# Optimization experiments

Measured on AMD Instinct MI355X. Metric: run time of the kernel, lower is better.

The kernel has to match this reference:

```python
import jax, jax.numpy as jnp
import numpy as np

SCALE = 0.125  # 1/sqrt(d_k), d_k = 64


def setup_inputs() -> dict:
    key = jax.random.key(0)
    kq, kk, kv, kp = jax.random.split(key, 4)
    H, B, L, T, D = 16, 4, 1024, 1024, 64
    return {
        "query": jax.random.normal(kq, (H, B, L, D), dtype=jnp.float32),
        "key": jax.random.normal(kk, (H, B, T, D), dtype=jnp.float32),
        "value": jax.random.normal(kv, (H, B, T, D), dtype=jnp.float32),
        "prev_attention": jax.random.normal(kp, (H, B, L, T), dtype=jnp.float32),
    }


def reference(query, key, value, prev_attention):
    # scores: [h, b, l, t]
    scores = jnp.einsum("hblk,hbtk->hblt", query, key) * SCALE
    scores = scores + prev_attention
    attention = jax.nn.softmax(scores, axis=-1)
    # dropout disabled (rate 0.0) for deterministic reference
    output = jnp.einsum("hblt,hbtv->hblv", attention, value)
    return (output, attention)
```

## Files before the change

### kernel.cpp

```cpp
#include <hip/hip_runtime.h>

#define SCALE 0.125f

constexpr int L_ = 1024, T_ = 1024, D_ = 64, HB_ = 64, QB = 16;

using f32x4  = __attribute__((ext_vector_type(4))) float;
using half8  = __attribute__((ext_vector_type(8))) _Float16;
using half4  = __attribute__((ext_vector_type(4))) _Float16;
using half2v = __attribute__((ext_vector_type(2))) _Float16;

#define BARRIER() asm volatile("s_waitcnt lgkmcnt(0)\n\ts_barrier" ::: "memory")

__global__ __launch_bounds__(256, 3) void attn_fused(
    const float* __restrict__ q, const float* __restrict__ kk,
    const float* __restrict__ vv, const float* __restrict__ prev,
    float* __restrict__ out, float* __restrict__ att) {
  __shared__ __align__(16) _Float16 El[QB][1032];
  __shared__ __align__(16) unsigned char KV[18432];
  __shared__ float zb[4][16];

  auto Ks  = (_Float16(*)[72])KV;
  auto Vt  = (_Float16(*)[72])(KV + 9216);
  auto ob4 = (float(*)[16][72])KV;

  const int ltile = blockIdx.x;
  const int hb    = blockIdx.y;
  const int tid = threadIdx.x;
  const int w = tid >> 6, l = tid & 63, l15 = l & 15, lg = l >> 4;
  const int qrow = ltile * QB + l15;

  half8 qb2[2];
  {
    const float* qp = q + ((size_t)hb * L_ + qrow) * D_ + lg * 8;
#pragma unroll
    for (int f = 0; f < 2; ++f)
#pragma unroll
      for (int e = 0; e < 8; ++e) qb2[f][e] = (_Float16)qp[f * 32 + e];
  }

  const float* prow =
      prev + ((size_t)hb * L_ + qrow) * (size_t)T_ + w * 16 + lg * 4;
  const float* kbase = kk + (size_t)hb * T_ * D_;
  const float* vbase = vv + (size_t)hb * T_ * D_;

  const int sr = tid >> 2;
  const int sc = (tid & 3) * 16;
  const int sv_d = (tid & 15) * 4;
  const int sv_t = (tid >> 4) * 4;

  f32x4 kq[2][4], vq[2][4];
  f32x4 pbv[2];
  auto kload = [&](int c, int s) {
    const float* p = kbase + (size_t)(c * 64 + sr) * D_ + sc;
#pragma unroll
    for (int i = 0; i < 4; ++i) kq[s][i] = *(const f32x4*)(p + i * 4);
  };
  auto vload = [&](int c, int s) {
    const float* p = vbase + (size_t)(c * 64 + sv_t) * D_ + sv_d;
#pragma unroll
    for (int j = 0; j < 4; ++j) vq[s][j] = *(const f32x4*)(p + j * D_);
  };
  auto pload = [&](int c, int s) { pbv[s] = *(const f32x4*)(prow + c * 64); };
  auto kwrite = [&](int s) {
    half8 h0, h1;
#pragma unroll
    for (int e = 0; e < 4; ++e) {
      h0[e]     = (_Float16)kq[s][0][e];
      h0[4 + e] = (_Float16)kq[s][1][e];
      h1[e]     = (_Float16)kq[s][2][e];
      h1[4 + e] = (_Float16)kq[s][3][e];
    }
    *(half8*)&Ks[sr][sc] = h0;
    *(half8*)&Ks[sr][sc + 8] = h1;
  };
  auto vwrite = [&](int s) {
#pragma unroll
    for (int dd = 0; dd < 4; ++dd) {
      half2v a, b;
      a[0] = (_Float16)vq[s][0][dd]; a[1] = (_Float16)vq[s][1][dd];
      b[0] = (_Float16)vq[s][2][dd]; b[1] = (_Float16)vq[s][3][dd];
      *(half2v*)&Vt[sv_d + dd][sv_t]     = a;
      *(half2v*)&Vt[sv_d + dd][sv_t + 2] = b;
    }
  };

  kload(0, 0); vload(0, 0); pload(0, 0);
  kwrite(0); vwrite(0);
  kload(1, 1); vload(1, 1); pload(1, 1);

  float zsum = 0.f;
  f32x4 oacc[4];
#pragma unroll
  for (int nd = 0; nd < 4; ++nd) oacc[nd] = (f32x4){0.f, 0.f, 0.f, 0.f};

#pragma unroll 2
  for (int c = 0; c < 16; ++c) {
    BARRIER();
    f32x4 pv = pbv[c & 1];
    if (c < 14) {
      kload(c + 2, c & 1);
      vload(c + 2, c & 1);
      pload(c + 2, c & 1);
    }

    __builtin_amdgcn_s_setprio(1);
    const int trow = w * 16 + l15;
    half8 ka0 = *(const half8*)&Ks[trow][lg * 8];
    half8 ka1 = *(const half8*)&Ks[trow][32 + lg * 8];
    f32x4 acc = {0.f, 0.f, 0.f, 0.f};
    acc = __builtin_amdgcn_mfma_f32_16x16x32_f16(ka0, qb2[0], acc, 0, 0, 0);
    acc = __builtin_amdgcn_mfma_f32_16x16x32_f16(ka1, qb2[1], acc, 0, 0, 0);

    float e0 = __expf(acc[0] * SCALE + pv[0]);
    float e1 = __expf(acc[1] * SCALE + pv[1]);
    float e2 = __expf(acc[2] * SCALE + pv[2]);
    float e3 = __expf(acc[3] * SCALE + pv[3]);
    zsum += (e0 + e1) + (e2 + e3);
    half4 ev;
    ev[0] = (_Float16)e0; ev[1] = (_Float16)e1;
    ev[2] = (_Float16)e2; ev[3] = (_Float16)e3;
    *(half4*)&El[l15][c * 64 + w * 16 + lg * 4] = ev;

    half8 af;
    af[0] = ev[0]; af[1] = ev[1]; af[2] = ev[2]; af[3] = ev[3];
    af[4] = af[5] = af[6] = af[7] = (_Float16)0.f;
#pragma unroll
    for (int nd = 0; nd < 4; ++nd) {
      half4 v4 = *(const half4*)&Vt[nd * 16 + l15][w * 16 + lg * 4];
      half8 vb;
      vb[0] = v4[0]; vb[1] = v4[1]; vb[2] = v4[2]; vb[3] = v4[3];
      vb[4] = vb[5] = vb[6] = vb[7] = (_Float16)0.f;
      oacc[nd] = __builtin_amdgcn_mfma_f32_16x16x32_f16(af, vb, oacc[nd], 0, 0, 0);
    }
    __builtin_amdgcn_s_setprio(0);

    BARRIER();
    if (c < 15) { kwrite((c + 1) & 1); vwrite((c + 1) & 1); }
  }

  zsum += __shfl_xor(zsum, 16, 64);
  zsum += __shfl_xor(zsum, 32, 64);
  if (lg == 0) zb[w][l15] = zsum;

#pragma unroll
  for (int nd = 0; nd < 4; ++nd)
#pragma unroll
    for (int i = 0; i < 4; ++i)
      ob4[w][lg * 4 + i][nd * 16 + l15] = oacc[nd][i];
  __syncthreads();

  {
    const int qq = tid >> 4, dd = (tid & 15) * 4;
    const float z = (zb[0][qq] + zb[1][qq]) + (zb[2][qq] + zb[3][qq]);
    const float rzq = 1.0f / z;
    f32x4 o0 = *(const f32x4*)&ob4[0][qq][dd];
    f32x4 o1 = *(const f32x4*)&ob4[1][qq][dd];
    f32x4 o2 = *(const f32x4*)&ob4[2][qq][dd];
    f32x4 o3 = *(const f32x4*)&ob4[3][qq][dd];
    f32x4 o = ((o0 + o1) + (o2 + o3));
    o[0] *= rzq; o[1] *= rzq; o[2] *= rzq; o[3] *= rzq;
    *(f32x4*)(out + ((size_t)hb * L_ + ltile * QB + qq) * (size_t)D_ + dd) = o;
  }

  {
    const int row = tid >> 4, tc = tid & 15;
    const float z = (zb[0][row] + zb[1][row]) + (zb[2][row] + zb[3][row]);
    const float rzr = 1.0f / z;
    float* attw =
        att + ((size_t)hb * L_ + ltile * QB + row) * (size_t)T_ + tc * 4;
    const _Float16* ep = &El[row][tc * 4];
#pragma unroll
    for (int j = 0; j < 16; ++j) {
      half4 ev = *(const half4*)(ep + j * 64);
      f32x4 s = {(float)ev[0] * rzr, (float)ev[1] * rzr,
                 (float)ev[2] * rzr, (float)ev[3] * rzr};
      *(f32x4*)(attw + j * 64) = s;
    }
  }
}

extern "C" void kernel_launch(void* const* d_in, const int* in_sizes, int n_in,
                              void* d_out, int out_size, void* d_ws,
                              size_t ws_size, hipStream_t stream) {
  const float* q    = (const float*)d_in[0];
  const float* k    = (const float*)d_in[1];
  const float* v    = (const float*)d_in[2];
  const float* prev = (const float*)d_in[3];

  float* out = (float*)d_out;
  float* att = out + (size_t)HB_ * L_ * D_;

  dim3 grid(L_ / QB, HB_);
  attn_fused<<<grid, 256, 0, stream>>>(q, k, v, prev, out, att);
}
```

Before: 248.5 us.

## Pre-convert K/V to fp16 in workspace and stream directly without LDS staging

Adds two pre-pass kernels that convert K to fp16 and V to a transposed fp16 layout in the workspace. The main kernel then reads K and V fragments straight from global memory (expected to hit L2) instead of staging them through shared memory, which removes the per-chunk barriers and LDS writes. The prev-attention prefetch is restructured into groups of four chunks. The trade-off is extra kernel launches and a workspace round-trip, plus dependence on L2/cache hit rates for the uncoalesced direct loads. The old fused kernel stays as a fallback when the workspace is too small.

```diff
diff --git a/kernel.cpp b/kernel.cpp
--- a/kernel.cpp
+++ b/kernel.cpp
@@ -11,17 +11,54 @@
 
 #define BARRIER() asm volatile("s_waitcnt lgkmcnt(0)\n\ts_barrier" ::: "memory")
 
-__global__ __launch_bounds__(256, 3) void attn_fused(
-    const float* __restrict__ q, const float* __restrict__ kk,
-    const float* __restrict__ vv, const float* __restrict__ prev,
+__global__ __launch_bounds__(256) void cvt_k(const float* __restrict__ k,
+                                             _Float16* __restrict__ kh) {
+  const size_t i = ((size_t)blockIdx.x * 256 + threadIdx.x) * 8;
+  f32x4 a = *(const f32x4*)(k + i);
+  f32x4 b = *(const f32x4*)(k + i + 4);
+  half8 h;
+#pragma unroll
+  for (int e = 0; e < 4; ++e) {
+    h[e] = (_Float16)a[e];
+    h[4 + e] = (_Float16)b[e];
+  }
+  *(half8*)(kh + i) = h;
+}
+
+__global__ __launch_bounds__(256) void cvt_v(const float* __restrict__ v,
+                                             _Float16* __restrict__ vh) {
+  __shared__ _Float16 ts[64][136];
+  const int tid = threadIdx.x;
+  const int hb = blockIdx.y;
+  const int t0 = blockIdx.x * 128;
+
+  {
+    const int tr = tid >> 1, dh = (tid & 1) * 32;
+    const float* p = v + ((size_t)hb * T_ + t0 + tr) * D_ + dh;
+#pragma unroll
+    for (int i = 0; i < 8; ++i) {
+      f32x4 r = *(const f32x4*)(p + i * 4);
+#pragma unroll
+      for (int e = 0; e < 4; ++e) ts[dh + i * 4 + e][tr] = (_Float16)r[e];
+    }
+  }
+  __syncthreads();
+  {
+    const int d = tid >> 2, tq = (tid & 3) * 32;
+    _Float16* qo = vh + ((size_t)hb * D_ + d) * T_ + t0 + tq;
+#pragma unroll
+    for (int i = 0; i < 4; ++i)
+      *(half8*)(qo + i * 8) = *(const half8*)&ts[d][tq + i * 8];
+  }
+}
+
+__global__ __launch_bounds__(256, 3) void attn_stream(
+    const float* __restrict__ q, const _Float16* __restrict__ Kh,
+    const _Float16* __restrict__ Vh, const float* __restrict__ prev,
     float* __restrict__ out, float* __restrict__ att) {
   __shared__ __align__(16) _Float16 El[QB][1032];
-  __shared__ __align__(16) unsigned char KV[18432];
-  __shared__ float zb[4][16];
-
-  auto Ks  = (_Float16(*)[72])KV;
-  auto Vt  = (_Float16(*)[72])(KV + 9216);
-  auto ob4 = (float(*)[16][72])KV;
+  __shared__ __align__(16) float ob4[4][QB][68];
+  __shared__ float zb[4][QB];
 
   const int ltile = blockIdx.x;
   const int hb    = blockIdx.y;
@@ -40,102 +77,65 @@
 
   const float* prow =
       prev + ((size_t)hb * L_ + qrow) * (size_t)T_ + w * 16 + lg * 4;
-  const float* kbase = kk + (size_t)hb * T_ * D_;
-  const float* vbase = vv + (size_t)hb * T_ * D_;
-
-  const int sr = tid >> 2;
-  const int sc = (tid & 3) * 16;
-  const int sv_d = (tid & 15) * 4;
-  const int sv_t = (tid >> 4) * 4;
-
-  f32x4 kq[2][4], vq[2][4];
-  f32x4 pbv[2];
-  auto kload = [&](int c, int s) {
-    const float* p = kbase + (size_t)(c * 64 + sr) * D_ + sc;
-#pragma unroll
-    for (int i = 0; i < 4; ++i) kq[s][i] = *(const f32x4*)(p + i * 4);
-  };
-  auto vload = [&](int c, int s) {
-    const float* p = vbase + (size_t)(c * 64 + sv_t) * D_ + sv_d;
-#pragma unroll
-    for (int j = 0; j < 4; ++j) vq[s][j] = *(const f32x4*)(p + j * D_);
-  };
-  auto pload = [&](int c, int s) { pbv[s] = *(const f32x4*)(prow + c * 64); };
-  auto kwrite = [&](int s) {
-    half8 h0, h1;
-#pragma unroll
-    for (int e = 0; e < 4; ++e) {
-      h0[e]     = (_Float16)kq[s][0][e];
-      h0[4 + e] = (_Float16)kq[s][1][e];
-      h1[e]     = (_Float16)kq[s][2][e];
-      h1[4 + e] = (_Float16)kq[s][3][e];
-    }
-    *(half8*)&Ks[sr][sc] = h0;
-    *(half8*)&Ks[sr][sc + 8] = h1;
-  };
-  auto vwrite = [&](int s) {
-#pragma unroll
-    for (int dd = 0; dd < 4; ++dd) {
-      half2v a, b;
-      a[0] = (_Float16)vq[s][0][dd]; a[1] = (_Float16)vq[s][1][dd];
-      b[0] = (_Float16)vq[s][2][dd]; b[1] = (_Float16)vq[s][3][dd];
-      *(half2v*)&Vt[sv_d + dd][sv_t]     = a;
-      *(half2v*)&Vt[sv_d + dd][sv_t + 2] = b;
-    }
-  };
-
-  kload(0, 0); vload(0, 0); pload(0, 0);
-  kwrite(0); vwrite(0);
-  kload(1, 1); vload(1, 1); pload(1, 1);
+  const _Float16* kb = Kh + (size_t)hb * T_ * D_;
+  const _Float16* vb = Vh + (size_t)hb * D_ * T_;
+
+  f32x4 pcur[4], pnext[4];
+#pragma unroll
+  for (int j = 0; j < 4; ++j) pcur[j] = *(const f32x4*)(prow + j * 64);
+#pragma unroll
+  for (int j = 0; j < 4; ++j) pnext[j] = *(const f32x4*)(prow + (4 + j) * 64);
 
   float zsum = 0.f;
   f32x4 oacc[4];
 #pragma unroll
   for (int nd = 0; nd < 4; ++nd) oacc[nd] = (f32x4){0.f, 0.f, 0.f, 0.f};
 
-#pragma unroll 2
-  for (int c = 0; c < 16; ++c) {
-    BARRIER();
-    f32x4 pv = pbv[c & 1];
-    if (c < 14) {
-      kload(c + 2, c & 1);
-      vload(c + 2, c & 1);
-      pload(c + 2, c & 1);
-    }
-
-    __builtin_amdgcn_s_setprio(1);
-    const int trow = w * 16 + l15;
-    half8 ka0 = *(const half8*)&Ks[trow][lg * 8];
-    half8 ka1 = *(const half8*)&Ks[trow][32 + lg * 8];
-    f32x4 acc = {0.f, 0.f, 0.f, 0.f};
-    acc = __builtin_amdgcn_mfma_f32_16x16x32_f16(ka0, qb2[0], acc, 0, 0, 0);
-    acc = __builtin_amdgcn_mfma_f32_16x16x32_f16(ka1, qb2[1], acc, 0, 0, 0);
-
-    float e0 = __expf(acc[0] * SCALE + pv[0]);
-    float e1 = __expf(acc[1] * SCALE + pv[1]);
-    float e2 = __expf(acc[2] * SCALE + pv[2]);
-    float e3 = __expf(acc[3] * SCALE + pv[3]);
-    zsum += (e0 + e1) + (e2 + e3);
-    half4 ev;
-    ev[0] = (_Float16)e0; ev[1] = (_Float16)e1;
-    ev[2] = (_Float16)e2; ev[3] = (_Float16)e3;
-    *(half4*)&El[l15][c * 64 + w * 16 + lg * 4] = ev;
-
-    half8 af;
-    af[0] = ev[0]; af[1] = ev[1]; af[2] = ev[2]; af[3] = ev[3];
-    af[4] = af[5] = af[6] = af[7] = (_Float16)0.f;
-#pragma unroll
-    for (int nd = 0; nd < 4; ++nd) {
-      half4 v4 = *(const half4*)&Vt[nd * 16 + l15][w * 16 + lg * 4];
-      half8 vb;
-      vb[0] = v4[0]; vb[1] = v4[1]; vb[2] = v4[2]; vb[3] = v4[3];
-      vb[4] = vb[5] = vb[6] = vb[7] = (_Float16)0.f;
-      oacc[nd] = __builtin_amdgcn_mfma_f32_16x16x32_f16(af, vb, oacc[nd], 0, 0, 0);
-    }
-    __builtin_amdgcn_s_setprio(0);
-
-    BARRIER();
-    if (c < 15) { kwrite((c + 1) & 1); vwrite((c + 1) & 1); }
+#pragma unroll
+  for (int g = 0; g < 4; ++g) {
+#pragma unroll
+    for (int j = 0; j < 4; ++j) {
+      const int c = g * 4 + j;
+      const f32x4 pv = pcur[j];
+
+      const int trow = c * 64 + w * 16 + l15;
+      half8 ka0 = *(const half8*)(kb + (size_t)trow * D_ + lg * 8);
+      half8 ka1 = *(const half8*)(kb + (size_t)trow * D_ + 32 + lg * 8);
+      f32x4 acc = {0.f, 0.f, 0.f, 0.f};
+      acc = __builtin_amdgcn_mfma_f32_16x16x32_f16(ka0, qb2[0], acc, 0, 0, 0);
+      acc = __builtin_amdgcn_mfma_f32_16x16x32_f16(ka1, qb2[1], acc, 0, 0, 0);
+
+      float e0 = __expf(acc[0] * SCALE + pv[0]);
+      float e1 = __expf(acc[1] * SCALE + pv[1]);
+      float e2 = __expf(acc[2] * SCALE + pv[2]);
+      float e3 = __expf(acc[3] * SCALE + pv[3]);
+      zsum += (e0 + e1) + (e2 + e3);
+      half4 ev;
+      ev[0] = (_Float16)e0; ev[1] = (_Float16)e1;
+      ev[2] = (_Float16)e2; ev[3] = (_Float16)e3;
+      *(half4*)&El[l15][c * 64 + w * 16 + lg * 4] = ev;
+
+      half8 af;
+      af[0] = ev[0]; af[1] = ev[1]; af[2] = ev[2]; af[3] = ev[3];
+      af[4] = af[5] = af[6] = af[7] = (_Float16)0.f;
+#pragma unroll
+      for (int nd = 0; nd < 4; ++nd) {
+        half4 v4 = *(const half4*)(vb + (size_t)(nd * 16 + l15) * T_ +
+                                   c * 64 + w * 16 + lg * 4);
+        half8 vfb;
+        vfb[0] = v4[0]; vfb[1] = v4[1]; vfb[2] = v4[2]; vfb[3] = v4[3];
+        vfb[4] = vfb[5] = vfb[6] = vfb[7] = (_Float16)0.f;
+        oacc[nd] =
+            __builtin_amdgcn_mfma_f32_16x16x32_f16(af, vfb, oacc[nd], 0, 0, 0);
+      }
+    }
+#pragma unroll
+    for (int j = 0; j < 4; ++j) pcur[j] = pnext[j];
+    if (g < 2) {
+#pragma unroll
+      for (int j = 0; j < 4; ++j)
+        pnext[j] = *(const f32x4*)(prow + ((g + 2) * 4 + j) * 64);
+    }
   }
 
   zsum += __shfl_xor(zsum, 16, 64);
@@ -147,6 +147,7 @@
 #pragma unroll
     for (int i = 0; i < 4; ++i)
       ob4[w][lg * 4 + i][nd * 16 + l15] = oacc[nd][i];
+
   __syncthreads();
 
   {
@@ -179,6 +180,172 @@
   }
 }
 
+__global__ __launch_bounds__(256, 3) void attn_fused(
+    const float* __restrict__ q, const float* __restrict__ kk,
+    const float* __restrict__ vv, const float* __restrict__ prev,
+    float* __restrict__ out, float* __restrict__ att) {
+  __shared__ __align__(16) _Float16 El[QB][1032];
+  __shared__ __align__(16) unsigned char KV[18432];
+  __shared__ float zb[4][16];
+
+  auto Ks  = (_Float16(*)[72])KV;
+  auto Vt  = (_Float16(*)[72])(KV + 9216);
+  auto ob4 = (float(*)[16][72])KV;
+
+  const int ltile = blockIdx.x;
+  const int hb    = blockIdx.y;
+  const int tid = threadIdx.x;
+  const int w = tid >> 6, l = tid & 63, l15 = l & 15, lg = l >> 4;
+  const int qrow = ltile * QB + l15;
+
+  half8 qb2[2];
+  {
+    const float* qp = q + ((size_t)hb * L_ + qrow) * D_ + lg * 8;
+#pragma unroll
+    for (int f = 0; f < 2; ++f)
+#pragma unroll
+      for (int e = 0; e < 8; ++e) qb2[f][e] = (_Float16)qp[f * 32 + e];
+  }
+
+  const float* prow =
+      prev + ((size_t)hb * L_ + qrow) * (size_t)T_ + w * 16 + lg * 4;
+  const float* kbase = kk + (size_t)hb * T_ * D_;
+  const float* vbase = vv + (size_t)hb * T_ * D_;
+
+  const int sr = tid >> 2;
+  const int sc = (tid & 3) * 16;
+  const int sv_d = (tid & 15) * 4;
+  const int sv_t = (tid >> 4) * 4;
+
+  f32x4 kq[2][4], vq[2][4];
+  f32x4 pbv[2];
+  auto kload = [&](int c, int s) {
+    const float* p = kbase + (size_t)(c * 64 + sr) * D_ + sc;
+#pragma unroll
+    for (int i = 0; i < 4; ++i) kq[s][i] = *(const f32x4*)(p + i * 4);
+  };
+  auto vload = [&](int c, int s) {
+    const float* p = vbase + (size_t)(c * 64 + sv_t) * D_ + sv_d;
+#pragma unroll
+    for (int j = 0; j < 4; ++j) vq[s][j] = *(const f32x4*)(p + j * D_);
+  };
+  auto pload = [&](int c, int s) { pbv[s] = *(const f32x4*)(prow + c * 64); };
+  auto kwrite = [&](int s) {
+    half8 h0, h1;
+#pragma unroll
+    for (int e = 0; e < 4; ++e) {
+      h0[e]     = (_Float16)kq[s][0][e];
+      h0[4 + e] = (_Float16)kq[s][1][e];
+      h1[e]     = (_Float16)kq[s][2][e];
+      h1[4 + e] = (_Float16)kq[s][3][e];
+    }
+    *(half8*)&Ks[sr][sc] = h0;
+    *(half8*)&Ks[sr][sc + 8] = h1;
+  };
+  auto vwrite = [&](int s) {
+#pragma unroll
+    for (int dd = 0; dd < 4; ++dd) {
+      half2v a, b;
+      a[0] = (_Float16)vq[s][0][dd]; a[1] = (_Float16)vq[s][1][dd];
+      b[0] = (_Float16)vq[s][2][dd]; b[1] = (_Float16)vq[s][3][dd];
+      *(half2v*)&Vt[sv_d + dd][sv_t]     = a;
+      *(half2v*)&Vt[sv_d + dd][sv_t + 2] = b;
+    }
+  };
+
+  kload(0, 0); vload(0, 0); pload(0, 0);
+  kwrite(0); vwrite(0);
+  kload(1, 1); vload(1, 1); pload(1, 1);
+
+  float zsum = 0.f;
+  f32x4 oacc[4];
+#pragma unroll
+  for (int nd = 0; nd < 4; ++nd) oacc[nd] = (f32x4){0.f, 0.f, 0.f, 0.f};
+
+#pragma unroll 2
+  for (int c = 0; c < 16; ++c) {
+    BARRIER();
+    f32x4 pv = pbv[c & 1];
+    if (c < 14) {
+      kload(c + 2, c & 1);
+      vload(c + 2, c & 1);
+      pload(c + 2, c & 1);
+    }
+
+    const int trow = w * 16 + l15;
+    half8 ka0 = *(const half8*)&Ks[trow][lg * 8];
+    half8 ka1 = *(const half8*)&Ks[trow][32 + lg * 8];
+    f32x4 acc = {0.f, 0.f, 0.f, 0.f};
+    acc = __builtin_amdgcn_mfma_f32_16x16x32_f16(ka0, qb2[0], acc, 0, 0, 0);
+    acc = __builtin_amdgcn_mfma_f32_16x16x32_f16(ka1, qb2[1], acc, 0, 0, 0);
+
+    float e0 = __expf(acc[0] * SCALE + pv[0]);
+    float e1 = __expf(acc[1] * SCALE + pv[1]);
+    float e2 = __expf(acc[2] * SCALE + pv[2]);
+    float e3 = __expf(acc[3] * SCALE + pv[3]);
+    zsum += (e0 + e1) + (e2 + e3);
+    half4 ev;
+    ev[0] = (_Float16)e0; ev[1] = (_Float16)e1;
+    ev[2] = (_Float16)e2; ev[3] = (_Float16)e3;
+    *(half4*)&El[l15][c * 64 + w * 16 + lg * 4] = ev;
+
+    half8 af;
+    af[0] = ev[0]; af[1] = ev[1]; af[2] = ev[2]; af[3] = ev[3];
+    af[4] = af[5] = af[6] = af[7] = (_Float16)0.f;
+#pragma unroll
+    for (int nd = 0; nd < 4; ++nd) {
+      half4 v4 = *(const half4*)&Vt[nd * 16 + l15][w * 16 + lg * 4];
+      half8 vfb;
+      vfb[0] = v4[0]; vfb[1] = v4[1]; vfb[2] = v4[2]; vfb[3] = v4[3];
+      vfb[4] = vfb[5] = vfb[6] = vfb[7] = (_Float16)0.f;
+      oacc[nd] = __builtin_amdgcn_mfma_f32_16x16x32_f16(af, vfb, oacc[nd], 0, 0, 0);
+    }
+
+    BARRIER();
+    if (c < 15) { kwrite((c + 1) & 1); vwrite((c + 1) & 1); }
+  }
+
+  zsum += __shfl_xor(zsum, 16, 64);
+  zsum += __shfl_xor(zsum, 32, 64);
+  if (lg == 0) zb[w][l15] = zsum;
+
+#pragma unroll
+  for (int nd = 0; nd < 4; ++nd)
+#pragma unroll
+    for (int i = 0; i < 4; ++i)
+      ob4[w][lg * 4 + i][nd * 16 + l15] = oacc[nd][i];
+  __syncthreads();
+
+  {
+    const int qq = tid >> 4, dd = (tid & 15) * 4;
+    const float z = (zb[0][qq] + zb[1][qq]) + (zb[2][qq] + zb[3][qq]);
+    const float rzq = 1.0f / z;
+    f32x4 o0 = *(const f32x4*)&ob4[0][qq][dd];
+    f32x4 o1 = *(const f32x4*)&ob4[1][qq][dd];
+    f32x4 o2 = *(const f32x4*)&ob4[2][qq][dd];
+    f32x4 o3 = *(const f32x4*)&ob4[3][qq][dd];
+    f32x4 o = ((o0 + o1) + (o2 + o3));
+    o[0] *= rzq; o[1] *= rzq; o[2] *= rzq; o[3] *= rzq;
+    *(f32x4*)(out + ((size_t)hb * L_ + ltile * QB + qq) * (size_t)D_ + dd) = o;
+  }
+
+  {
+    const int row = tid >> 4, tc = tid & 15;
+    const float z = (zb[0][row] + zb[1][row]) + (zb[2][row] + zb[3][row]);
+    const float rzr = 1.0f / z;
+    float* attw =
+        att + ((size_t)hb * L_ + ltile * QB + row) * (size_t)T_ + tc * 4;
+    const _Float16* ep = &El[row][tc * 4];
+#pragma unroll
+    for (int j = 0; j < 16; ++j) {
+      half4 ev = *(const half4*)(ep + j * 64);
+      f32x4 s = {(float)ev[0] * rzr, (float)ev[1] * rzr,
+                 (float)ev[2] * rzr, (float)ev[3] * rzr};
+      *(f32x4*)(attw + j * 64) = s;
+    }
+  }
+}
+
 extern "C" void kernel_launch(void* const* d_in, const int* in_sizes, int n_in,
                               void* d_out, int out_size, void* d_ws,
                               size_t ws_size, hipStream_t stream) {
@@ -190,6 +357,17 @@
   float* out = (float*)d_out;
   float* att = out + (size_t)HB_ * L_ * D_;
 
-  dim3 grid(L_ / QB, HB_);
-  attn_fused<<<grid, 256, 0, stream>>>(q, k, v, prev, out, att);
-}
+  const size_t KV_ELEMS = (size_t)HB_ * T_ * D_;
+  const size_t WS_NEED  = 2 * KV_ELEMS * sizeof(_Float16);
+
+  if (ws_size >= WS_NEED) {
+    _Float16* Kh = (_Float16*)d_ws;
+    _Float16* Vh = Kh + KV_ELEMS;
+    cvt_k<<<(int)(KV_ELEMS / (256 * 8)), 256, 0, stream>>>(k, Kh);
+    cvt_v<<<dim3(T_ / 128, HB_), 256, 0, stream>>>(v, Vh);
+    attn_stream<<<dim3(L_ / QB, HB_), 256, 0, stream>>>(q, Kh, Vh, prev, out,
+                                                        att);
+  } else {
+    attn_fused<<<dim3(L_ / QB, HB_), 256, 0, stream>>>(q, k, v, prev, out, att);
+  }
+}
```

Result: slower. 294.3 us (+18.5%).
